# Kernel optimization log

Hardware: AMD Instinct MI355X
Metric: run time of the kernel (lower is better)

## Reference

```python
import jax, jax.numpy as jnp
import numpy as np

B, D, K0, K1 = 262144, 128, 50, 1  # batch, embed dim, cluster-space k, noise-space k


def setup_inputs() -> dict:
    key = jax.random.key(0)
    k_z, k_v, k_c0, k_c1 = jax.random.split(key, 4)
    z = jax.random.normal(k_z, (B, D), dtype=jnp.float32)
    # beta_weights_init with P=[range(0,64), range(64,128)], high_value=0.9
    high = 0.9
    on = np.float32(np.log(1.0 / high - 1.0))
    off = np.float32(np.log(1.0 / (1.0 - high) - 1.0))
    bw = np.full((2, D), off, dtype=np.float32)
    bw[0, : D // 2] = on
    bw[1, D // 2 :] = on
    beta_weights = jnp.asarray(bw)
    # orthogonal rotation matrix V (ENRC assumption: V^T V = I)
    V, _ = jnp.linalg.qr(jax.random.normal(k_v, (D, D), dtype=jnp.float32))
    centers0 = jax.random.normal(k_c0, (K0, D), dtype=jnp.float32)
    centers1 = jax.random.normal(k_c1, (K1, D), dtype=jnp.float32)
    return {"z": z, "beta_weights": beta_weights, "V": V,
            "centers0": centers0, "centers1": centers1}


def _weighted_sqdist(z_rot, centers, beta):
    # sum_d beta_d * (z_d - c_d)^2  =  (z^2)·beta + (c^2)·beta - 2 (z*beta) @ c^T
    zz = (z_rot * z_rot) @ beta          # [B]
    cc = (centers * centers) @ beta      # [K]
    cross = (z_rot * beta) @ centers.T   # [B, K]
    return zz[:, None] + cc[None, :] - 2.0 * cross


def reference(z, beta_weights, V, centers0, centers1):
    # soft subspace dimension assignments (softmax over sub-clusterings)
    betas = jax.nn.softmax(beta_weights, axis=0)      # [2, D]
    z_rot = z @ V                                     # rotate embeddings, [B, D]
    d0 = _weighted_sqdist(z_rot, centers0, betas[0])  # [B, K0]
    d1 = _weighted_sqdist(z_rot, centers1, betas[1])  # [B, K1]
    return jnp.concatenate([d0, d1], axis=1)          # [B, K0+K1]
```

## Files before the change

### kernel.cpp

```cpp
#include <hip/hip_runtime.h>
#include <hip/hip_bf16.h>

#define D     128
#define K0    50
#define NCOL  51
#define NT    12
#define TB    64

typedef __attribute__((ext_vector_type(4))) float  f32x4;
typedef __attribute__((ext_vector_type(8))) short  short8x;

__device__ inline short f2bf(float x) {
    __hip_bfloat16 h = __float2bfloat16(x);
    return __builtin_bit_cast(short, h);
}
__device__ inline float bf2f(short s) {
    union { unsigned u; float f; } cv;
    cv.u = ((unsigned)(unsigned short)s) << 16;
    return cv.f;
}

__global__ __launch_bounds__(128) void setup_kernel(
    const float* __restrict__ bw,
    const float* __restrict__ V,
    const float* __restrict__ c0,
    const float* __restrict__ c1,
    short* __restrict__ Gws,
    float* __restrict__ ccws)
{
    const int blk = blockIdx.x;
    const int t   = threadIdx.x;
    __shared__ float beta0[D];
    __shared__ float Vd[32][D];
    __shared__ float Bn[16][D];

    if (t < D) {
        float b0 = bw[t], b1 = bw[D + t];
        beta0[t] = 1.0f / (1.0f + expf(b1 - b0));
    }

    if (blk == 48) {
        __syncthreads();
        if (t < NCOL) {
            const float* cr = (t < K0) ? (c0 + (size_t)t * D) : c1;
            float s = 0.f;
            for (int e = 0; e < D; ++e) {
                float b = beta0[e];
                if (t == K0) b = 1.0f - b;
                float cv = cr[e];
                s += b * cv * cv;
            }
            ccws[t] = s;
        }
        return;
    }

    const int kstep = blk / NT;
    const int ntile = blk % NT;

    for (int i = t; i < 32 * (D / 4); i += 128)
        ((f32x4*)Vd)[i] = ((const f32x4*)(V + (size_t)kstep * 32 * D))[i];
    for (int i = t; i < 16 * (D / 4); i += 128) {
        int r = i / (D / 4);
        int n = ntile * 16 + r;
        f32x4 v;
        if (n < D)            v = ((const f32x4*)(V + (size_t)n * D))[i % (D / 4)];
        else if (n - D < K0)  v = ((const f32x4*)(c0 + (size_t)(n - D) * D))[i % (D / 4)];
        else if (n - D == K0) v = ((const f32x4*)c1)[i % (D / 4)];
        else                  v = f32x4{0.f, 0.f, 0.f, 0.f};
        ((f32x4*)Bn)[i] = v;
    }
    __syncthreads();

    const int lane  = t >> 1;
    const int jbase = (t & 1) * 4;
    const int nl    = lane & 15;
    const int n     = ntile * 16 + nl;
    const bool useB1 = (n == D + K0);
    short res[4];
    for (int jj = 0; jj < 4; ++jj) {
        int dl = (lane >> 4) * 8 + jbase + jj;
        float s = 0.f;
        #pragma unroll 8
        for (int e = 0; e < D; ++e) {
            float b = useB1 ? (1.0f - beta0[e]) : beta0[e];
            s += Vd[dl][e] * b * Bn[nl][e];
        }
        res[jj] = f2bf(s);
    }
    short* dst = Gws + ((size_t)(blk * 64 + lane)) * 8 + jbase;
    for (int jj = 0; jj < 4; ++jj) dst[jj] = res[jj];
}

__global__ __launch_bounds__(256, 2) void main_kernel(
    const float* __restrict__ z,
    const short* __restrict__ Gws,
    const float* __restrict__ ccws,
    float* __restrict__ out)
{
    __shared__ __align__(16) short Gs[4 * NT * 64 * 8];
    __shared__ __align__(16) short zbf[TB][D];

    const int t    = threadIdx.x;
    const int wave = t >> 6;
    const int lane = t & 63;
    const int c    = lane & 15;
    const int q    = lane >> 4;
    const size_t rowbase = (size_t)blockIdx.x * TB;

    for (int i = t; i < 4 * NT * 64 * 8 / 8; i += 256)
        ((int4*)Gs)[i] = ((const int4*)Gws)[i];

    const int arow = wave * 16 + c;
    const float* zrow = z + (rowbase + arow) * D;
    short8x afrag[4];
    #pragma unroll
    for (int ks = 0; ks < 4; ++ks) {
        const float* p = zrow + ks * 32 + q * 8;
        f32x4 v0 = *(const f32x4*)p;
        f32x4 v1 = *(const f32x4*)(p + 4);
        short8x a;
        a[0] = f2bf(v0.x); a[1] = f2bf(v0.y); a[2] = f2bf(v0.z); a[3] = f2bf(v0.w);
        a[4] = f2bf(v1.x); a[5] = f2bf(v1.y); a[6] = f2bf(v1.z); a[7] = f2bf(v1.w);
        afrag[ks] = a;
        *(short8x*)(&zbf[arow][ks * 32 + q * 8]) = a;
    }
    __syncthreads();

    f32x4 acc[NT];
    #pragma unroll
    for (int nt = 0; nt < NT; ++nt) acc[nt] = f32x4{0.f, 0.f, 0.f, 0.f};
    #pragma unroll
    for (int ks = 0; ks < 4; ++ks) {
        #pragma unroll
        for (int nt = 0; nt < NT; ++nt) {
            short8x bfrg = *(const short8x*)&Gs[((ks * NT + nt) * 64 + lane) * 8];
            acc[nt] = __builtin_amdgcn_mfma_f32_16x16x32_bf16(afrag[ks], bfrg, acc[nt], 0, 0, 0);
        }
    }

    float qp[4] = {0.f, 0.f, 0.f, 0.f};
    float np[4] = {0.f, 0.f, 0.f, 0.f};
    #pragma unroll
    for (int nt = 0; nt < 8; ++nt) {
        #pragma unroll
        for (int r = 0; r < 4; ++r) {
            float zv = bf2f(zbf[wave * 16 + q * 4 + r][nt * 16 + c]);
            qp[r] += zv * acc[nt][r];
            np[r] += zv * zv;
        }
    }
    #pragma unroll
    for (int s = 1; s < 16; s <<= 1) {
        #pragma unroll
        for (int r = 0; r < 4; ++r) {
            qp[r] += __shfl_xor(qp[r], s, 64);
            np[r] += __shfl_xor(np[r], s, 64);
        }
    }

    #pragma unroll
    for (int nt = 8; nt < NT; ++nt) {
        int k = (nt - 8) * 16 + c;
        if (k <= K0) {
            float ccv = ccws[k];
            #pragma unroll
            for (int r = 0; r < 4; ++r) {
                size_t row = rowbase + wave * 16 + q * 4 + r;
                float zz = (k < K0) ? qp[r] : (np[r] - qp[r]);
                out[row * NCOL + k] = zz + ccv - 2.0f * acc[nt][r];
            }
        }
    }
}

extern "C" void kernel_launch(void* const* d_in, const int* in_sizes, int n_in,
                              void* d_out, int out_size, void* d_ws, size_t ws_size,
                              hipStream_t stream) {
    const float* z  = (const float*)d_in[0];
    const float* bw = (const float*)d_in[1];
    const float* V  = (const float*)d_in[2];
    const float* c0 = (const float*)d_in[3];
    const float* c1 = (const float*)d_in[4];
    float* out = (float*)d_out;

    short* Gws  = (short*)d_ws;
    float* ccws = (float*)((char*)d_ws + 4 * NT * 64 * 8 * 2);

    const int B = in_sizes[0] / D;

    setup_kernel<<<49, 128, 0, stream>>>(bw, V, c0, c1, Gws, ccws);
    main_kernel<<<B / TB, 256, 0, stream>>>(z, Gws, ccws, out);
}
```

Before: 241.3 us.

## Use rotated outputs directly for norms and process multiple row tiles per block

The weighted norm is now computed from the rotated vector itself: the MFMA output y = z@V is squared and weighted by beta in registers, instead of reading back a bf16 copy of z from shared memory. The zbf shared buffer disappears. Each block now handles 256 rows by looping four row tiles per wave, which amortises the load of the G matrix into shared memory, and launch bounds are raised to 3 blocks per SM. The setup kernel is restructured with transposed shared layouts and writes beta to the workspace. The trade-off is more serial work per block and fewer blocks overall.

Result: slower. 349.3 us (+44.7%).

```diff
diff --git a/kernel.cpp b/kernel.cpp
--- a/kernel.cpp
+++ b/kernel.cpp
@@ -5,7 +5,7 @@
 #define K0    50
 #define NCOL  51
 #define NT    12
-#define TB    64
+#define TB    256
 
 typedef __attribute__((ext_vector_type(4))) float  f32x4;
 typedef __attribute__((ext_vector_type(8))) short  short8x;
@@ -13,11 +13,6 @@
 __device__ inline short f2bf(float x) {
     __hip_bfloat16 h = __float2bfloat16(x);
     return __builtin_bit_cast(short, h);
-}
-__device__ inline float bf2f(short s) {
-    union { unsigned u; float f; } cv;
-    cv.u = ((unsigned)(unsigned short)s) << 16;
-    return cv.f;
 }
 
 __global__ __launch_bounds__(128) void setup_kernel(
@@ -26,27 +21,28 @@
     const float* __restrict__ c0,
     const float* __restrict__ c1,
     short* __restrict__ Gws,
-    float* __restrict__ ccws)
+    float* __restrict__ ccws,
+    float* __restrict__ betaws)
 {
     const int blk = blockIdx.x;
     const int t   = threadIdx.x;
     __shared__ float beta0[D];
-    __shared__ float Vd[32][D];
-    __shared__ float Bn[16][D];
+    __shared__ float Vt[D * 33];
+    __shared__ float wct[D * 17];
 
     if (t < D) {
         float b0 = bw[t], b1 = bw[D + t];
         beta0[t] = 1.0f / (1.0f + expf(b1 - b0));
     }
+    __syncthreads();
 
     if (blk == 48) {
-        __syncthreads();
+        if (t < D) betaws[t] = beta0[t];
         if (t < NCOL) {
             const float* cr = (t < K0) ? (c0 + (size_t)t * D) : c1;
             float s = 0.f;
             for (int e = 0; e < D; ++e) {
-                float b = beta0[e];
-                if (t == K0) b = 1.0f - b;
+                float b = (t == K0) ? (1.0f - beta0[e]) : beta0[e];
                 float cv = cr[e];
                 s += b * cv * cv;
             }
@@ -57,49 +53,55 @@
 
     const int kstep = blk / NT;
     const int ntile = blk % NT;
-
-    for (int i = t; i < 32 * (D / 4); i += 128)
-        ((f32x4*)Vd)[i] = ((const f32x4*)(V + (size_t)kstep * 32 * D))[i];
-    for (int i = t; i < 16 * (D / 4); i += 128) {
-        int r = i / (D / 4);
-        int n = ntile * 16 + r;
-        f32x4 v;
-        if (n < D)            v = ((const f32x4*)(V + (size_t)n * D))[i % (D / 4)];
-        else if (n - D < K0)  v = ((const f32x4*)(c0 + (size_t)(n - D) * D))[i % (D / 4)];
-        else if (n - D == K0) v = ((const f32x4*)c1)[i % (D / 4)];
-        else                  v = f32x4{0.f, 0.f, 0.f, 0.f};
-        ((f32x4*)Bn)[i] = v;
-    }
-    __syncthreads();
-
     const int lane  = t >> 1;
     const int jbase = (t & 1) * 4;
     const int nl    = lane & 15;
-    const int n     = ntile * 16 + nl;
-    const bool useB1 = (n == D + K0);
+
+    if (ntile < 8) {
+        const int n = ntile * 16 + nl;
+        short* dst = Gws + ((size_t)(blk * 64 + lane)) * 8 + jbase;
+        for (int jj = 0; jj < 4; ++jj) {
+            int d = kstep * 32 + (lane >> 4) * 8 + jbase + jj;
+            dst[jj] = f2bf(V[(size_t)d * D + n]);
+        }
+        return;
+    }
+
+    for (int i = t; i < 32 * D; i += 128) {
+        int d = i >> 7, e = i & 127;
+        Vt[e * 33 + d] = V[(size_t)(kstep * 32 + d) * D + e];
+    }
+    for (int i = t; i < 16 * D; i += 128) {
+        int kl = i >> 7, e = i & 127;
+        int k = (ntile - 8) * 16 + kl;
+        float w = 0.f;
+        if (k < K0)       w = beta0[e] * c0[(size_t)k * D + e];
+        else if (k == K0) w = (1.0f - beta0[e]) * c1[e];
+        wct[e * 17 + kl] = w;
+    }
+    __syncthreads();
+
     short res[4];
     for (int jj = 0; jj < 4; ++jj) {
         int dl = (lane >> 4) * 8 + jbase + jj;
         float s = 0.f;
         #pragma unroll 8
-        for (int e = 0; e < D; ++e) {
-            float b = useB1 ? (1.0f - beta0[e]) : beta0[e];
-            s += Vd[dl][e] * b * Bn[nl][e];
-        }
+        for (int e = 0; e < D; ++e)
+            s += Vt[e * 33 + dl] * wct[e * 17 + nl];
         res[jj] = f2bf(s);
     }
     short* dst = Gws + ((size_t)(blk * 64 + lane)) * 8 + jbase;
     for (int jj = 0; jj < 4; ++jj) dst[jj] = res[jj];
 }
 
-__global__ __launch_bounds__(256, 2) void main_kernel(
+__global__ __launch_bounds__(256, 3) void main_kernel(
     const float* __restrict__ z,
     const short* __restrict__ Gws,
     const float* __restrict__ ccws,
+    const float* __restrict__ betaws,
     float* __restrict__ out)
 {
-    __shared__ __align__(16) short Gs[4 * NT * 64 * 8];
-    __shared__ __align__(16) short zbf[TB][D];
+    __shared__ __align__(16) short Gs[48 * 64 * 8];
 
     const int t    = threadIdx.x;
     const int wave = t >> 6;
@@ -108,67 +110,79 @@
     const int q    = lane >> 4;
     const size_t rowbase = (size_t)blockIdx.x * TB;
 
-    for (int i = t; i < 4 * NT * 64 * 8 / 8; i += 256)
+    for (int i = t; i < 48 * 64 * 8 / 8; i += 256)
         ((int4*)Gs)[i] = ((const int4*)Gws)[i];
 
-    const int arow = wave * 16 + c;
-    const float* zrow = z + (rowbase + arow) * D;
-    short8x afrag[4];
+    float breg[8];
     #pragma unroll
-    for (int ks = 0; ks < 4; ++ks) {
-        const float* p = zrow + ks * 32 + q * 8;
-        f32x4 v0 = *(const f32x4*)p;
-        f32x4 v1 = *(const f32x4*)(p + 4);
-        short8x a;
-        a[0] = f2bf(v0.x); a[1] = f2bf(v0.y); a[2] = f2bf(v0.z); a[3] = f2bf(v0.w);
-        a[4] = f2bf(v1.x); a[5] = f2bf(v1.y); a[6] = f2bf(v1.z); a[7] = f2bf(v1.w);
-        afrag[ks] = a;
-        *(short8x*)(&zbf[arow][ks * 32 + q * 8]) = a;
+    for (int nt = 0; nt < 8; ++nt) breg[nt] = betaws[nt * 16 + c];
+    float creg[4];
+    #pragma unroll
+    for (int j = 0; j < 4; ++j) {
+        int kk = j * 16 + c;
+        creg[j] = (kk <= K0) ? ccws[kk] : 0.f;
     }
     __syncthreads();
 
-    f32x4 acc[NT];
-    #pragma unroll
-    for (int nt = 0; nt < NT; ++nt) acc[nt] = f32x4{0.f, 0.f, 0.f, 0.f};
-    #pragma unroll
-    for (int ks = 0; ks < 4; ++ks) {
-        #pragma unroll
-        for (int nt = 0; nt < NT; ++nt) {
-            short8x bfrg = *(const short8x*)&Gs[((ks * NT + nt) * 64 + lane) * 8];
-            acc[nt] = __builtin_amdgcn_mfma_f32_16x16x32_bf16(afrag[ks], bfrg, acc[nt], 0, 0, 0);
-        }
-    }
-
-    float qp[4] = {0.f, 0.f, 0.f, 0.f};
-    float np[4] = {0.f, 0.f, 0.f, 0.f};
-    #pragma unroll
-    for (int nt = 0; nt < 8; ++nt) {
-        #pragma unroll
-        for (int r = 0; r < 4; ++r) {
-            float zv = bf2f(zbf[wave * 16 + q * 4 + r][nt * 16 + c]);
-            qp[r] += zv * acc[nt][r];
-            np[r] += zv * zv;
-        }
-    }
-    #pragma unroll
-    for (int s = 1; s < 16; s <<= 1) {
-        #pragma unroll
-        for (int r = 0; r < 4; ++r) {
-            qp[r] += __shfl_xor(qp[r], s, 64);
-            np[r] += __shfl_xor(np[r], s, 64);
-        }
-    }
-
-    #pragma unroll
-    for (int nt = 8; nt < NT; ++nt) {
-        int k = (nt - 8) * 16 + c;
-        if (k <= K0) {
-            float ccv = ccws[k];
+    for (int rt = 0; rt < 4; ++rt) {
+        const int rowloc = (wave * 4 + rt) * 16;
+        const float* zrow = z + (rowbase + rowloc + c) * D;
+
+        short8x afrag[4];
+        #pragma unroll
+        for (int ks = 0; ks < 4; ++ks) {
+            const float* p = zrow + ks * 32 + q * 8;
+            f32x4 v0 = *(const f32x4*)p;
+            f32x4 v1 = *(const f32x4*)(p + 4);
+            short8x a;
+            a[0] = f2bf(v0.x); a[1] = f2bf(v0.y); a[2] = f2bf(v0.z); a[3] = f2bf(v0.w);
+            a[4] = f2bf(v1.x); a[5] = f2bf(v1.y); a[6] = f2bf(v1.z); a[7] = f2bf(v1.w);
+            afrag[ks] = a;
+        }
+
+        f32x4 acc[NT];
+        #pragma unroll
+        for (int nt = 0; nt < NT; ++nt) acc[nt] = f32x4{0.f, 0.f, 0.f, 0.f};
+        #pragma unroll
+        for (int ks = 0; ks < 4; ++ks) {
+            #pragma unroll
+            for (int nt = 0; nt < NT; ++nt) {
+                short8x bfrg = *(const short8x*)&Gs[((ks * NT + nt) * 64 + lane) * 8];
+                acc[nt] = __builtin_amdgcn_mfma_f32_16x16x32_bf16(afrag[ks], bfrg, acc[nt], 0, 0, 0);
+            }
+        }
+
+        float qp[4] = {0.f, 0.f, 0.f, 0.f};
+        float np_[4] = {0.f, 0.f, 0.f, 0.f};
+        #pragma unroll
+        for (int nt = 0; nt < 8; ++nt) {
             #pragma unroll
             for (int r = 0; r < 4; ++r) {
-                size_t row = rowbase + wave * 16 + q * 4 + r;
-                float zz = (k < K0) ? qp[r] : (np[r] - qp[r]);
-                out[row * NCOL + k] = zz + ccv - 2.0f * acc[nt][r];
+                float y = acc[nt][r];
+                float y2 = y * y;
+                np_[r] += y2;
+                qp[r] += breg[nt] * y2;
+            }
+        }
+        #pragma unroll
+        for (int s = 1; s < 16; s <<= 1) {
+            #pragma unroll
+            for (int r = 0; r < 4; ++r) {
+                qp[r]  += __shfl_xor(qp[r], s, 64);
+                np_[r] += __shfl_xor(np_[r], s, 64);
+            }
+        }
+
+        const size_t rowg = rowbase + rowloc + q * 4;
+        #pragma unroll
+        for (int j = 0; j < 4; ++j) {
+            int kk = j * 16 + c;
+            if (kk <= K0) {
+                #pragma unroll
+                for (int r = 0; r < 4; ++r) {
+                    float zz = (kk < K0) ? qp[r] : (np_[r] - qp[r]);
+                    out[(rowg + r) * NCOL + kk] = zz + creg[j] - 2.0f * acc[8 + j][r];
+                }
             }
         }
     }
@@ -184,11 +198,12 @@
     const float* c1 = (const float*)d_in[4];
     float* out = (float*)d_out;
 
-    short* Gws  = (short*)d_ws;
-    float* ccws = (float*)((char*)d_ws + 4 * NT * 64 * 8 * 2);
+    short* Gws    = (short*)d_ws;
+    float* ccws   = (float*)((char*)d_ws + 48 * 64 * 8 * 2);
+    float* betaws = ccws + 64;
 
     const int B = in_sizes[0] / D;
 
-    setup_kernel<<<49, 128, 0, stream>>>(bw, V, c0, c1, Gws, ccws);
-    main_kernel<<<B / TB, 256, 0, stream>>>(z, Gws, ccws, out);
-}
+    setup_kernel<<<49, 128, 0, stream>>>(bw, V, c0, c1, Gws, ccws, betaws);
+    main_kernel<<<B / TB, 256, 0, stream>>>(z, Gws, ccws, betaws, out);
+}
```
